# Kernel tuning notes

Measured on AMD Instinct MI355X. Metric: run time of the kernel, lower is better.

Reference implementation:

```python
import jax, jax.numpy as jnp
import numpy as np

B, S, D, E, K, FF = 4, 2048, 1024, 8, 2, 4096  # batch, seq, d_model, experts, top-k, 4*d_model


def setup_inputs() -> dict:
    key = jax.random.key(0)
    k0, k1, k2, k3 = jax.random.split(key, 4)
    scale = 0.02
    return {
        "x": jax.random.normal(k0, (B, S, D), jnp.float32),
        "gate_w": jax.random.normal(k1, (D, E), jnp.float32) * scale,
        "w1": jax.random.normal(k2, (E, D, FF), jnp.float32) * scale,
        "b1": jnp.zeros((E, FF), jnp.float32),
        "w2": jax.random.normal(k3, (E, FF, D), jnp.float32) * scale,
        "b2": jnp.zeros((E, D), jnp.float32),
    }


def reference(x, gate_w, w1, b1, w2, b2):
    # Gating: top-k logits, softmax over the selected k (matches torch.topk + softmax)
    logits = jnp.einsum("bsd,de->bse", x, gate_w)  # [B,S,E]
    vals, idxs = jax.lax.top_k(logits, K)           # [B,S,K]
    w = jax.nn.softmax(vals, axis=-1)               # [B,S,K]
    n_exp = gate_w.shape[-1]
    # Per-token combine weight for each expert (0 if not selected)
    combine = jnp.sum(jax.nn.one_hot(idxs, n_exp, dtype=x.dtype) * w[..., None], axis=-2)  # [B,S,E]

    out = jnp.zeros_like(x)
    for e in range(n_exp):  # fixed small loop over experts
        h = jax.nn.silu(jnp.einsum("bsd,df->bsf", x, w1[e]) + b1[e])  # dropout = identity (eval)
        y = jnp.einsum("bsf,fd->bsd", h, w2[e]) + b2[e]
        out = out + combine[..., e:e + 1] * y
    return out
```

## Files before the change

kernel.cpp:

```cpp
#include <hip/hip_runtime.h>
#include <math.h>

#define Tt 8192
#define Dd 1024
#define Ee 8
#define FFf 4096
#define SLOTS (Tt*2)

typedef unsigned short u16;
typedef unsigned int u32;
typedef __attribute__((ext_vector_type(8))) __bf16 bf16x8;
typedef __attribute__((ext_vector_type(4))) float f32x4;

__device__ __forceinline__ u16 f2bf(float f) {
  union { float f; u32 u; } v; v.f = f;
  u32 u = v.u;
  return (u16)((u + 0x7FFFu + ((u >> 16) & 1u)) >> 16);
}
__device__ __forceinline__ float bf2f(u16 h) {
  union { u32 u; float f; } v; v.u = ((u32)h) << 16; return v.f;
}
__device__ __forceinline__ void gl2lds16(const u16* g, u16* l) {
  __builtin_amdgcn_global_load_lds((const __attribute__((address_space(1))) void*)g,
                                   (__attribute__((address_space(3))) void*)l, 16, 0, 0);
}

__global__ void gate_topk_kernel(const float* __restrict__ x,
                                 const float* __restrict__ gw,
                                 int* __restrict__ counts,
                                 int* __restrict__ tok_e,
                                 float* __restrict__ tok_w,
                                 u16* __restrict__ xb) {
  int wave = (int)((blockIdx.x * blockDim.x + threadIdx.x) >> 6);
  int lane = threadIdx.x & 63;
  if (wave >= Tt) return;
  const float* xrow = x + (size_t)wave * Dd;
  int d0 = lane * 16;
  const f32x4* xr4 = (const f32x4*)(xrow + d0);
  f32x4 v0 = xr4[0], v1 = xr4[1], v2 = xr4[2], v3 = xr4[3];
  float xv[16];
#pragma unroll
  for (int k = 0; k < 4; k++) { xv[k] = v0[k]; xv[4 + k] = v1[k]; xv[8 + k] = v2[k]; xv[12 + k] = v3[k]; }
  float p[Ee];
#pragma unroll
  for (int e = 0; e < Ee; e++) p[e] = 0.f;
#pragma unroll
  for (int i = 0; i < 16; i++) {
    const float* g = gw + (size_t)(d0 + i) * Ee;
#pragma unroll
    for (int e = 0; e < Ee; e++) p[e] += xv[i] * g[e];
  }
  {
    uint4 o0, o1;
    o0.x = (u32)f2bf(xv[0]) | ((u32)f2bf(xv[1]) << 16);
    o0.y = (u32)f2bf(xv[2]) | ((u32)f2bf(xv[3]) << 16);
    o0.z = (u32)f2bf(xv[4]) | ((u32)f2bf(xv[5]) << 16);
    o0.w = (u32)f2bf(xv[6]) | ((u32)f2bf(xv[7]) << 16);
    o1.x = (u32)f2bf(xv[8]) | ((u32)f2bf(xv[9]) << 16);
    o1.y = (u32)f2bf(xv[10]) | ((u32)f2bf(xv[11]) << 16);
    o1.z = (u32)f2bf(xv[12]) | ((u32)f2bf(xv[13]) << 16);
    o1.w = (u32)f2bf(xv[14]) | ((u32)f2bf(xv[15]) << 16);
    u16* dp = xb + (size_t)wave * Dd + d0;
    *(uint4*)dp = o0;
    *(uint4*)(dp + 8) = o1;
  }
#pragma unroll
  for (int e = 0; e < Ee; e++) {
    for (int off = 32; off > 0; off >>= 1) p[e] += __shfl_xor(p[e], off, 64);
  }
  if (lane == 0) {
    int e0 = 0; float v0s = p[0];
#pragma unroll
    for (int e = 1; e < Ee; e++) if (p[e] > v0s) { v0s = p[e]; e0 = e; }
    int e1 = -1; float v1s = -INFINITY;
#pragma unroll
    for (int e = 0; e < Ee; e++) if (e != e0 && p[e] > v1s) { v1s = p[e]; e1 = e; }
    float w0 = 1.f / (1.f + expf(v1s - v0s));
    float w1 = 1.f - w0;
    tok_e[wave * 2 + 0] = e0; tok_e[wave * 2 + 1] = e1;
    tok_w[wave * 2 + 0] = w0; tok_w[wave * 2 + 1] = w1;
    atomicAdd(&counts[e0], 1);
    atomicAdd(&counts[e1], 1);
  }
}

__global__ __launch_bounds__(256) void wconv_kernel(const float* __restrict__ src,
                                                    u16* __restrict__ dst, int R, int C) {
  __shared__ float t[64][65];
  int e = blockIdx.z;
  size_t ebase = (size_t)e * R * C;
  int r0 = blockIdx.y * 64, c0 = blockIdx.x * 64;
  int tid = threadIdx.x;
  int row = tid >> 2, q = tid & 3;
  const float* sp = src + ebase + (size_t)(r0 + row) * C + c0 + q * 16;
  f32x4 v0 = *(const f32x4*)(sp);
  f32x4 v1 = *(const f32x4*)(sp + 4);
  f32x4 v2 = *(const f32x4*)(sp + 8);
  f32x4 v3 = *(const f32x4*)(sp + 12);
#pragma unroll
  for (int k = 0; k < 4; k++) t[row][q * 16 + k] = v0[k];
#pragma unroll
  for (int k = 0; k < 4; k++) t[row][q * 16 + 4 + k] = v1[k];
#pragma unroll
  for (int k = 0; k < 4; k++) t[row][q * 16 + 8 + k] = v2[k];
#pragma unroll
  for (int k = 0; k < 4; k++) t[row][q * 16 + 12 + k] = v3[k];
  __syncthreads();
  float c[16];
#pragma unroll
  for (int k = 0; k < 16; k++) c[k] = t[q * 16 + k][row];
  uint4 d0, d1;
  d0.x = (u32)f2bf(c[0]) | ((u32)f2bf(c[1]) << 16);
  d0.y = (u32)f2bf(c[2]) | ((u32)f2bf(c[3]) << 16);
  d0.z = (u32)f2bf(c[4]) | ((u32)f2bf(c[5]) << 16);
  d0.w = (u32)f2bf(c[6]) | ((u32)f2bf(c[7]) << 16);
  d1.x = (u32)f2bf(c[8]) | ((u32)f2bf(c[9]) << 16);
  d1.y = (u32)f2bf(c[10]) | ((u32)f2bf(c[11]) << 16);
  d1.z = (u32)f2bf(c[12]) | ((u32)f2bf(c[13]) << 16);
  d1.w = (u32)f2bf(c[14]) | ((u32)f2bf(c[15]) << 16);
  u16* dp = dst + ebase + (size_t)(c0 + row) * R + r0 + q * 16;
  *(uint4*)dp = d0;
  *(uint4*)(dp + 8) = d1;
}

__global__ void scan_kernel(const int* __restrict__ counts,
                            int* __restrict__ offsets, int* __restrict__ cursors) {
  if (threadIdx.x == 0 && blockIdx.x == 0) {
    int acc = 0;
    for (int e = 0; e < Ee; e++) { offsets[e] = acc; cursors[e] = acc; acc += counts[e]; }
  }
}

__global__ void scatter_kernel(const int* __restrict__ tok_e, const float* __restrict__ tok_w,
                               int* __restrict__ cursors,
                               int* __restrict__ slot_token, float* __restrict__ slot_w,
                               int* __restrict__ tok_slot) {
  int t = blockIdx.x * blockDim.x + threadIdx.x;
  if (t >= Tt) return;
#pragma unroll
  for (int k = 0; k < 2; k++) {
    int e = tok_e[t * 2 + k];
    int pos = atomicAdd(&cursors[e], 1);
    slot_token[pos] = t;
    slot_w[pos] = tok_w[t * 2 + k];
    tok_slot[t * 2 + k] = pos;
  }
}

#define MFMA16(H)                                                                 \
  do {                                                                            \
    acc[H][0][0] = __builtin_amdgcn_mfma_f32_16x16x32_bf16(a0, b0, acc[H][0][0], 0, 0, 0); \
    acc[H][0][1] = __builtin_amdgcn_mfma_f32_16x16x32_bf16(a0, b1, acc[H][0][1], 0, 0, 0); \
    acc[H][0][2] = __builtin_amdgcn_mfma_f32_16x16x32_bf16(a0, b2, acc[H][0][2], 0, 0, 0); \
    acc[H][0][3] = __builtin_amdgcn_mfma_f32_16x16x32_bf16(a0, b3, acc[H][0][3], 0, 0, 0); \
    acc[H][1][0] = __builtin_amdgcn_mfma_f32_16x16x32_bf16(a1, b0, acc[H][1][0], 0, 0, 0); \
    acc[H][1][1] = __builtin_amdgcn_mfma_f32_16x16x32_bf16(a1, b1, acc[H][1][1], 0, 0, 0); \
    acc[H][1][2] = __builtin_amdgcn_mfma_f32_16x16x32_bf16(a1, b2, acc[H][1][2], 0, 0, 0); \
    acc[H][1][3] = __builtin_amdgcn_mfma_f32_16x16x32_bf16(a1, b3, acc[H][1][3], 0, 0, 0); \
    acc[H][2][0] = __builtin_amdgcn_mfma_f32_16x16x32_bf16(a2, b0, acc[H][2][0], 0, 0, 0); \
    acc[H][2][1] = __builtin_amdgcn_mfma_f32_16x16x32_bf16(a2, b1, acc[H][2][1], 0, 0, 0); \
    acc[H][2][2] = __builtin_amdgcn_mfma_f32_16x16x32_bf16(a2, b2, acc[H][2][2], 0, 0, 0); \
    acc[H][2][3] = __builtin_amdgcn_mfma_f32_16x16x32_bf16(a2, b3, acc[H][2][3], 0, 0, 0); \
    acc[H][3][0] = __builtin_amdgcn_mfma_f32_16x16x32_bf16(a3, b0, acc[H][3][0], 0, 0, 0); \
    acc[H][3][1] = __builtin_amdgcn_mfma_f32_16x16x32_bf16(a3, b1, acc[H][3][1], 0, 0, 0); \
    acc[H][3][2] = __builtin_amdgcn_mfma_f32_16x16x32_bf16(a3, b2, acc[H][3][2], 0, 0, 0); \
    acc[H][3][3] = __builtin_amdgcn_mfma_f32_16x16x32_bf16(a3, b3, acc[H][3][3], 0, 0, 0); \
  } while (0)

template<int KDIM, int NDIM, int EPI, int GATHER>
__device__ __forceinline__ void moe_body(
    const u16* __restrict__ A, const u16* __restrict__ BT,
    const float* __restrict__ bias,
    const int* __restrict__ offsets, const int* __restrict__ counts,
    const int* __restrict__ slot_token, const float* __restrict__ slot_w,
    u16* __restrict__ O16, float* __restrict__ Of) {
  constexpr int NT = KDIM / 64;
  int e = blockIdx.z;
  int cnt = counts[e];
  int rb = blockIdx.y;
  if (rb * 256 >= cnt) return;
  int off = offsets[e];
  int n0 = blockIdx.x * 256;

  __shared__ u16 S[65536];

  int tid = threadIdx.x;
  int lane = tid & 63, wave = tid >> 6;
  int wr = wave >> 2, wc = wave & 3;
  int lr = lane & 15, g = lane >> 4;

  const u16* BTe = BT + (size_t)e * NDIM * KDIM;

  const u16* aSrc[2][2];
  const u16* bSrc[2][2];
  int amax = off + cnt - 1;
#pragma unroll
  for (int h = 0; h < 2; h++)
#pragma unroll
    for (int s = 0; s < 2; s++) {
      int c = tid + s * 512;
      int lc = c ^ (((c >> 5) & 1) << 1);
      int ks = lc >> 9, rl = (lc >> 2) & 127, seg = lc & 3;
      int slotRow = off + rb * 256 + h * 128 + rl;
      if (slotRow > amax) slotRow = amax;
      int arow = GATHER ? slot_token[slotRow] : slotRow;
      aSrc[h][s] = A + (size_t)arow * KDIM + ks * 32 + seg * 8;
    }
#pragma unroll
  for (int ks = 0; ks < 2; ks++)
#pragma unroll
    for (int s = 0; s < 2; s++) {
      int c = tid + s * 512;
      int lc = c ^ (((c >> 5) & 1) << 1);
      int row = lc >> 2, seg = lc & 3;
      bSrc[ks][s] = BTe + (size_t)(n0 + row) * KDIM + ks * 32 + seg * 8;
    }

  auto stA = [&](int u, int h) {
    u16* d = &S[(u & 1) * 16384 + h * 8192 + wave * 512];
    gl2lds16(aSrc[h][0] + (size_t)u * 64, d);
    gl2lds16(aSrc[h][1] + (size_t)u * 64, d + 4096);
  };
  auto stB = [&](int u, int ks) {
    u16* d = &S[32768 + (u & 1) * 16384 + ks * 8192 + wave * 512];
    gl2lds16(bSrc[ks][0] + (size_t)u * 64, d);
    gl2lds16(bSrc[ks][1] + (size_t)u * 64, d + 4096);
  };
  auto rdA = [&](int dbuf, int hm, int ks, int i) -> bf16x8 {
    int rl = wr * 64 + i * 16 + lr;
    int logb = ks * 8192 + rl * 64 + g * 16;
    int phys = logb ^ (((rl >> 3) & 1) << 5);
    return *reinterpret_cast<const bf16x8*>(&S[dbuf * 16384 + hm * 8192 + (phys >> 1)]);
  };
  auto rdB = [&](int dbuf, int ks, int j) -> bf16x8 {
    int row = wc * 64 + j * 16 + lr;
    int logb = row * 64 + g * 16;
    int phys = logb ^ (((row >> 3) & 1) << 5);
    return *reinterpret_cast<const bf16x8*>(&S[32768 + dbuf * 16384 + ks * 8192 + (phys >> 1)]);
  };

  f32x4 acc[2][4][4];
#pragma unroll
  for (int h = 0; h < 2; h++)
#pragma unroll
    for (int i = 0; i < 4; i++)
#pragma unroll
      for (int j = 0; j < 4; j++) acc[h][i][j] = (f32x4)(0.0f);

  stB(0, 0); stA(0, 0); stA(0, 1); stB(0, 1);
  stB(1, 0); stA(1, 0);
  asm volatile("s_waitcnt vmcnt(4)" ::: "memory");
  __builtin_amdgcn_s_barrier();

  bf16x8 b0, b1, b2, b3;
  for (int t = 0; t < NT; ++t) {
    int dbuf = t & 1;
    {
      bf16x8 a0 = rdA(dbuf, 0, 0, 0), a1 = rdA(dbuf, 0, 0, 1),
             a2 = rdA(dbuf, 0, 0, 2), a3 = rdA(dbuf, 0, 0, 3);
      b0 = rdB(dbuf, 0, 0); b1 = rdB(dbuf, 0, 1); b2 = rdB(dbuf, 0, 2); b3 = rdB(dbuf, 0, 3);
      if (t + 1 < NT) stA(t + 1, 1);
      __builtin_amdgcn_s_barrier();
      asm volatile("s_waitcnt lgkmcnt(0)" ::: "memory");
      __builtin_amdgcn_sched_barrier(0);
      __builtin_amdgcn_s_setprio(1);
      MFMA16(0);
      __builtin_amdgcn_s_setprio(0);
      __builtin_amdgcn_s_barrier();
    }
    {
      bf16x8 a0 = rdA(dbuf, 1, 0, 0), a1 = rdA(dbuf, 1, 0, 1),
             a2 = rdA(dbuf, 1, 0, 2), a3 = rdA(dbuf, 1, 0, 3);
      if (t + 1 < NT) {
        stB(t + 1, 1);
        asm volatile("s_waitcnt vmcnt(6)" ::: "memory");
      }
      __builtin_amdgcn_s_barrier();
      asm volatile("s_waitcnt lgkmcnt(0)" ::: "memory");
      __builtin_amdgcn_sched_barrier(0);
      __builtin_amdgcn_s_setprio(1);
      MFMA16(1);
      __builtin_amdgcn_s_setprio(0);
      __builtin_amdgcn_s_barrier();
    }
    {
      bf16x8 a0 = rdA(dbuf, 0, 1, 0), a1 = rdA(dbuf, 0, 1, 1),
             a2 = rdA(dbuf, 0, 1, 2), a3 = rdA(dbuf, 0, 1, 3);
      b0 = rdB(dbuf, 1, 0); b1 = rdB(dbuf, 1, 1); b2 = rdB(dbuf, 1, 2); b3 = rdB(dbuf, 1, 3);
      if (t + 2 < NT) stB(t + 2, 0);
      __builtin_amdgcn_s_barrier();
      asm volatile("s_waitcnt lgkmcnt(0)" ::: "memory");
      __builtin_amdgcn_sched_barrier(0);
      __builtin_amdgcn_s_setprio(1);
      MFMA16(0);
      __builtin_amdgcn_s_setprio(0);
      __builtin_amdgcn_s_barrier();
    }
    {
      bf16x8 a0 = rdA(dbuf, 1, 1, 0), a1 = rdA(dbuf, 1, 1, 1),
             a2 = rdA(dbuf, 1, 1, 2), a3 = rdA(dbuf, 1, 1, 3);
      if (t + 2 < NT) {
        stA(t + 2, 0);
        asm volatile("s_waitcnt vmcnt(6)" ::: "memory");
      } else if (t + 1 < NT) {
        asm volatile("s_waitcnt vmcnt(0)" ::: "memory");
      }
      __builtin_amdgcn_s_barrier();
      asm volatile("s_waitcnt lgkmcnt(0)" ::: "memory");
      __builtin_amdgcn_sched_barrier(0);
      __builtin_amdgcn_s_setprio(1);
      MFMA16(1);
      __builtin_amdgcn_s_setprio(0);
      __builtin_amdgcn_s_barrier();
    }
  }

  int rlim = cnt - rb * 256;
#pragma unroll
  for (int hm = 0; hm < 2; hm++)
#pragma unroll
    for (int i = 0; i < 4; i++)
#pragma unroll
      for (int q = 0; q < 4; q++) {
        int m = hm * 128 + wr * 64 + i * 16 + g * 4 + q;
        if (m < rlim) {
          int slot = off + rb * 256 + m;
#pragma unroll
          for (int j = 0; j < 4; j++) {
            int n = n0 + wc * 64 + j * 16 + lr;
            float v = acc[hm][i][j][q] + bias[e * NDIM + n];
            if (EPI == 0) {
              float sv = v / (1.f + expf(-v));
              O16[(size_t)slot * NDIM + n] = f2bf(sv);
            } else if (EPI == 1) {
              O16[(size_t)slot * NDIM + n] = f2bf(v * slot_w[slot]);
            } else {
              atomicAdd(Of + (size_t)slot_token[slot] * NDIM + n, v * slot_w[slot]);
            }
          }
        }
      }
}

__global__ __launch_bounds__(512, 2) void moe_g1_kernel(
    const u16* __restrict__ A, const u16* __restrict__ BT, const float* __restrict__ bias,
    const int* __restrict__ offsets, const int* __restrict__ counts,
    const int* __restrict__ slot_token, const float* __restrict__ slot_w,
    u16* __restrict__ O16) {
  moe_body<Dd, FFf, 0, 1>(A, BT, bias, offsets, counts, slot_token, slot_w, O16, nullptr);
}
__global__ __launch_bounds__(512, 2) void moe_g2_kernel(
    const u16* __restrict__ A, const u16* __restrict__ BT, const float* __restrict__ bias,
    const int* __restrict__ offsets, const int* __restrict__ counts,
    const int* __restrict__ slot_token, const float* __restrict__ slot_w,
    u16* __restrict__ O16) {
  moe_body<FFf, Dd, 1, 0>(A, BT, bias, offsets, counts, slot_token, slot_w, O16, nullptr);
}
__global__ __launch_bounds__(512, 2) void moe_g2_atomic_kernel(
    const u16* __restrict__ A, const u16* __restrict__ BT, const float* __restrict__ bias,
    const int* __restrict__ offsets, const int* __restrict__ counts,
    const int* __restrict__ slot_token, const float* __restrict__ slot_w,
    float* __restrict__ Of) {
  moe_body<FFf, Dd, 2, 0>(A, BT, bias, offsets, counts, slot_token, slot_w, nullptr, Of);
}

__global__ void combine_kernel(const u16* __restrict__ y, const int* __restrict__ tok_slot,
                               float* __restrict__ out) {
  int gid = blockIdx.x * blockDim.x + threadIdx.x;
  int t = gid >> 7;
  int seg = gid & 127;
  int s0 = tok_slot[t * 2 + 0], s1 = tok_slot[t * 2 + 1];
  uint4 a = *(const uint4*)(y + (size_t)s0 * Dd + seg * 8);
  uint4 b = *(const uint4*)(y + (size_t)s1 * Dd + seg * 8);
  f32x4 o0, o1;
  o0[0] = bf2f((u16)a.x) + bf2f((u16)b.x);
  o0[1] = bf2f((u16)(a.x >> 16)) + bf2f((u16)(b.x >> 16));
  o0[2] = bf2f((u16)a.y) + bf2f((u16)b.y);
  o0[3] = bf2f((u16)(a.y >> 16)) + bf2f((u16)(b.y >> 16));
  o1[0] = bf2f((u16)a.z) + bf2f((u16)b.z);
  o1[1] = bf2f((u16)(a.z >> 16)) + bf2f((u16)(b.z >> 16));
  o1[2] = bf2f((u16)a.w) + bf2f((u16)b.w);
  o1[3] = bf2f((u16)(a.w >> 16)) + bf2f((u16)(b.w >> 16));
  float* op = out + (size_t)t * Dd + seg * 8;
  *(f32x4*)op = o0;
  *(f32x4*)(op + 4) = o1;
}

extern "C" void kernel_launch(void* const* d_in, const int* in_sizes, int n_in,
                              void* d_out, int out_size, void* d_ws, size_t ws_size,
                              hipStream_t stream) {
  const float* x  = (const float*)d_in[0];
  const float* gw = (const float*)d_in[1];
  const float* w1 = (const float*)d_in[2];
  const float* b1 = (const float*)d_in[3];
  const float* w2 = (const float*)d_in[4];
  const float* b2 = (const float*)d_in[5];
  float* out = (float*)d_out;

  char* ws = (char*)d_ws;
  size_t off_counts = 0;
  size_t off_offsets = 256;
  size_t off_cursors = 512;
  size_t off_tok_e = 1024;
  size_t off_tok_w     = off_tok_e + (size_t)Tt * 2 * 4;
  size_t off_tok_slot  = off_tok_w + (size_t)Tt * 2 * 4;
  size_t off_slot_token= off_tok_slot + (size_t)Tt * 2 * 4;
  size_t off_slot_w    = off_slot_token + (size_t)SLOTS * 4;
  size_t off_xb        = off_slot_w + (size_t)SLOTS * 4;
  size_t off_h         = off_xb + (size_t)Tt * Dd * 2;
  size_t off_wT        = off_h + (size_t)SLOTS * FFf * 2;
  size_t off_y         = off_wT + (size_t)Ee * Dd * FFf * 2;
  size_t need_atomic   = off_y;
  size_t need_full     = off_y + (size_t)SLOTS * Dd * 2;
  if (ws_size < need_atomic) return;
  int use_combine = (ws_size >= need_full) ? 1 : 0;

  int* counts     = (int*)(ws + off_counts);
  int* offsets    = (int*)(ws + off_offsets);
  int* cursors    = (int*)(ws + off_cursors);
  int* tok_e      = (int*)(ws + off_tok_e);
  float* tok_w    = (float*)(ws + off_tok_w);
  int* tok_slot   = (int*)(ws + off_tok_slot);
  int* slot_token = (int*)(ws + off_slot_token);
  float* slot_w   = (float*)(ws + off_slot_w);
  u16* xb         = (u16*)(ws + off_xb);
  u16* h          = (u16*)(ws + off_h);
  u16* wT         = (u16*)(ws + off_wT);
  u16* y          = (u16*)(ws + off_y);

  hipMemsetAsync(ws, 0, 1024, stream);

  gate_topk_kernel<<<Tt / 4, 256, 0, stream>>>(x, gw, counts, tok_e, tok_w, xb);
  scan_kernel<<<1, 64, 0, stream>>>(counts, offsets, cursors);
  scatter_kernel<<<Tt / 256, 256, 0, stream>>>(tok_e, tok_w, cursors, slot_token, slot_w, tok_slot);

  {
    dim3 gc(FFf / 64, Dd / 64, Ee);
    wconv_kernel<<<gc, 256, 0, stream>>>(w1, wT, Dd, FFf);
  }
  {
    dim3 g1(FFf / 256, Tt / 256, Ee);
    moe_g1_kernel<<<g1, 512, 0, stream>>>(xb, wT, b1, offsets, counts,
                                          slot_token, slot_w, h);
  }
  {
    dim3 gc(Dd / 64, FFf / 64, Ee);
    wconv_kernel<<<gc, 256, 0, stream>>>(w2, wT, FFf, Dd);
  }
  if (use_combine) {
    dim3 g2(Dd / 256, Tt / 256, Ee);
    moe_g2_kernel<<<g2, 512, 0, stream>>>(h, wT, b2, offsets, counts,
                                          slot_token, slot_w, y);
    combine_kernel<<<(Tt * 128) / 256, 256, 0, stream>>>(y, tok_slot, out);
  } else {
    hipMemsetAsync(d_out, 0, (size_t)out_size * sizeof(float), stream);
    dim3 g2(Dd / 256, Tt / 256, Ee);
    moe_g2_atomic_kernel<<<g2, 512, 0, stream>>>(h, wT, b2, offsets, counts,
                                                 slot_token, slot_w, out);
  }
}
```

Baseline: 786.0 us.

## Split second MoE GEMM along K into two halves and combine partials

Adds a split-K variant of the down-projection GEMM. Each block handles half of the FF reduction dimension and writes a separate bf16 partial output buffer, and a new combine kernel sums four partials per token (two slots times two halves). This doubles the grid of the second GEMM, which otherwise has only 4 column tiles per expert and row block, to improve CU occupancy. In exchange it writes and reads an extra partial buffer and adds an extra bf16 rounding of the partials. It only runs when the workspace is large enough.

```diff
diff --git a/kernel.cpp b/kernel.cpp
--- a/kernel.cpp
+++ b/kernel.cpp
@@ -173,11 +173,10 @@
     const float* __restrict__ bias,
     const int* __restrict__ offsets, const int* __restrict__ counts,
     const int* __restrict__ slot_token, const float* __restrict__ slot_w,
-    u16* __restrict__ O16, float* __restrict__ Of) {
-  constexpr int NT = KDIM / 64;
+    u16* __restrict__ O16, float* __restrict__ Of,
+    int rb, int kbase, int ntiles) {
   int e = blockIdx.z;
   int cnt = counts[e];
-  int rb = blockIdx.y;
   if (rb * 256 >= cnt) return;
   int off = offsets[e];
   int n0 = blockIdx.x * 256;
@@ -204,7 +203,7 @@
       int slotRow = off + rb * 256 + h * 128 + rl;
       if (slotRow > amax) slotRow = amax;
       int arow = GATHER ? slot_token[slotRow] : slotRow;
-      aSrc[h][s] = A + (size_t)arow * KDIM + ks * 32 + seg * 8;
+      aSrc[h][s] = A + (size_t)arow * KDIM + kbase + ks * 32 + seg * 8;
     }
 #pragma unroll
   for (int ks = 0; ks < 2; ks++)
@@ -213,7 +212,7 @@
       int c = tid + s * 512;
       int lc = c ^ (((c >> 5) & 1) << 1);
       int row = lc >> 2, seg = lc & 3;
-      bSrc[ks][s] = BTe + (size_t)(n0 + row) * KDIM + ks * 32 + seg * 8;
+      bSrc[ks][s] = BTe + (size_t)(n0 + row) * KDIM + kbase + ks * 32 + seg * 8;
     }
 
   auto stA = [&](int u, int h) {
@@ -247,6 +246,7 @@
 #pragma unroll
       for (int j = 0; j < 4; j++) acc[h][i][j] = (f32x4)(0.0f);
 
+  const int NT = ntiles;
   stB(0, 0); stA(0, 0); stA(0, 1); stB(0, 1);
   stB(1, 0); stA(1, 0);
   asm volatile("s_waitcnt vmcnt(4)" ::: "memory");
@@ -328,7 +328,8 @@
 #pragma unroll
           for (int j = 0; j < 4; j++) {
             int n = n0 + wc * 64 + j * 16 + lr;
-            float v = acc[hm][i][j][q] + bias[e * NDIM + n];
+            float v = acc[hm][i][j][q];
+            if (bias != nullptr) v += bias[e * NDIM + n];
             if (EPI == 0) {
               float sv = v / (1.f + expf(-v));
               O16[(size_t)slot * NDIM + n] = f2bf(sv);
@@ -347,21 +348,34 @@
     const int* __restrict__ offsets, const int* __restrict__ counts,
     const int* __restrict__ slot_token, const float* __restrict__ slot_w,
     u16* __restrict__ O16) {
-  moe_body<Dd, FFf, 0, 1>(A, BT, bias, offsets, counts, slot_token, slot_w, O16, nullptr);
+  moe_body<Dd, FFf, 0, 1>(A, BT, bias, offsets, counts, slot_token, slot_w, O16, nullptr,
+                          blockIdx.y, 0, Dd / 64);
+}
+__global__ __launch_bounds__(512, 2) void moe_g2s_kernel(
+    const u16* __restrict__ A, const u16* __restrict__ BT, const float* __restrict__ bias,
+    const int* __restrict__ offsets, const int* __restrict__ counts,
+    const int* __restrict__ slot_token, const float* __restrict__ slot_w,
+    u16* __restrict__ y) {
+  int ksp = blockIdx.y & 1;
+  moe_body<FFf, Dd, 1, 0>(A, BT, ksp ? nullptr : bias, offsets, counts, slot_token, slot_w,
+                          y + (size_t)ksp * SLOTS * Dd, nullptr,
+                          blockIdx.y >> 1, ksp * (FFf / 2), FFf / 128);
 }
 __global__ __launch_bounds__(512, 2) void moe_g2_kernel(
     const u16* __restrict__ A, const u16* __restrict__ BT, const float* __restrict__ bias,
     const int* __restrict__ offsets, const int* __restrict__ counts,
     const int* __restrict__ slot_token, const float* __restrict__ slot_w,
     u16* __restrict__ O16) {
-  moe_body<FFf, Dd, 1, 0>(A, BT, bias, offsets, counts, slot_token, slot_w, O16, nullptr);
+  moe_body<FFf, Dd, 1, 0>(A, BT, bias, offsets, counts, slot_token, slot_w, O16, nullptr,
+                          blockIdx.y, 0, FFf / 64);
 }
 __global__ __launch_bounds__(512, 2) void moe_g2_atomic_kernel(
     const u16* __restrict__ A, const u16* __restrict__ BT, const float* __restrict__ bias,
     const int* __restrict__ offsets, const int* __restrict__ counts,
     const int* __restrict__ slot_token, const float* __restrict__ slot_w,
     float* __restrict__ Of) {
-  moe_body<FFf, Dd, 2, 0>(A, BT, bias, offsets, counts, slot_token, slot_w, nullptr, Of);
+  moe_body<FFf, Dd, 2, 0>(A, BT, bias, offsets, counts, slot_token, slot_w, nullptr, Of,
+                          blockIdx.y, 0, FFf / 64);
 }
 
 __global__ void combine_kernel(const u16* __restrict__ y, const int* __restrict__ tok_slot,
@@ -386,6 +400,31 @@
   *(f32x4*)(op + 4) = o1;
 }
 
+__global__ void combine4_kernel(const u16* __restrict__ y, const int* __restrict__ tok_slot,
+                                float* __restrict__ out) {
+  int gid = blockIdx.x * blockDim.x + threadIdx.x;
+  int t = gid >> 7;
+  int seg = gid & 127;
+  int s0 = tok_slot[t * 2 + 0], s1 = tok_slot[t * 2 + 1];
+  const u16* y1 = y + (size_t)SLOTS * Dd;
+  uint4 a = *(const uint4*)(y  + (size_t)s0 * Dd + seg * 8);
+  uint4 b = *(const uint4*)(y1 + (size_t)s0 * Dd + seg * 8);
+  uint4 c = *(const uint4*)(y  + (size_t)s1 * Dd + seg * 8);
+  uint4 d = *(const uint4*)(y1 + (size_t)s1 * Dd + seg * 8);
+  f32x4 o0, o1;
+  o0[0] = bf2f((u16)a.x) + bf2f((u16)b.x) + bf2f((u16)c.x) + bf2f((u16)d.x);
+  o0[1] = bf2f((u16)(a.x >> 16)) + bf2f((u16)(b.x >> 16)) + bf2f((u16)(c.x >> 16)) + bf2f((u16)(d.x >> 16));
+  o0[2] = bf2f((u16)a.y) + bf2f((u16)b.y) + bf2f((u16)c.y) + bf2f((u16)d.y);
+  o0[3] = bf2f((u16)(a.y >> 16)) + bf2f((u16)(b.y >> 16)) + bf2f((u16)(c.y >> 16)) + bf2f((u16)(d.y >> 16));
+  o1[0] = bf2f((u16)a.z) + bf2f((u16)b.z) + bf2f((u16)c.z) + bf2f((u16)d.z);
+  o1[1] = bf2f((u16)(a.z >> 16)) + bf2f((u16)(b.z >> 16)) + bf2f((u16)(c.z >> 16)) + bf2f((u16)(d.z >> 16));
+  o1[2] = bf2f((u16)a.w) + bf2f((u16)b.w) + bf2f((u16)c.w) + bf2f((u16)d.w);
+  o1[3] = bf2f((u16)(a.w >> 16)) + bf2f((u16)(b.w >> 16)) + bf2f((u16)(c.w >> 16)) + bf2f((u16)(d.w >> 16));
+  float* op = out + (size_t)t * Dd + seg * 8;
+  *(f32x4*)op = o0;
+  *(f32x4*)(op + 4) = o1;
+}
+
 extern "C" void kernel_launch(void* const* d_in, const int* in_sizes, int n_in,
                               void* d_out, int out_size, void* d_ws, size_t ws_size,
                               hipStream_t stream) {
@@ -411,9 +450,10 @@
   size_t off_wT        = off_h + (size_t)SLOTS * FFf * 2;
   size_t off_y         = off_wT + (size_t)Ee * Dd * FFf * 2;
   size_t need_atomic   = off_y;
-  size_t need_full     = off_y + (size_t)SLOTS * Dd * 2;
+  size_t need_y1       = off_y + (size_t)SLOTS * Dd * 2;
+  size_t need_y2       = off_y + (size_t)SLOTS * Dd * 2 * 2;
   if (ws_size < need_atomic) return;
-  int use_combine = (ws_size >= need_full) ? 1 : 0;
+  int tier = (ws_size >= need_y2) ? 2 : (ws_size >= need_y1) ? 1 : 0;
 
   int* counts     = (int*)(ws + off_counts);
   int* offsets    = (int*)(ws + off_offsets);
@@ -447,7 +487,12 @@
     dim3 gc(Dd / 64, FFf / 64, Ee);
     wconv_kernel<<<gc, 256, 0, stream>>>(w2, wT, FFf, Dd);
   }
-  if (use_combine) {
+  if (tier == 2) {
+    dim3 g2(Dd / 256, (Tt / 256) * 2, Ee);
+    moe_g2s_kernel<<<g2, 512, 0, stream>>>(h, wT, b2, offsets, counts,
+                                           slot_token, slot_w, y);
+    combine4_kernel<<<(Tt * 128) / 256, 256, 0, stream>>>(y, tok_slot, out);
+  } else if (tier == 1) {
     dim3 g2(Dd / 256, Tt / 256, Ee);
     moe_g2_kernel<<<g2, 512, 0, stream>>>(h, wT, b2, offsets, counts,
                                           slot_token, slot_w, y);
```

Result: slower. 850.4 us (+8.2%).
